# Kernel tuning notes

Measured on AMD Instinct MI355X. Metric: run time of the kernel, lower is better.

The kernel has to match this reference:

```python
import jax, jax.numpy as jnp
import numpy as np
from jax import lax

K = 3          # kernel_size
PAD = 1
D = 2 * K - 2  # 4 trajectory directions
C_IN = 64
C_OUT = 128


def setup_inputs() -> dict:
    key = jax.random.key(0)
    k1, k2, k3, k4, k5 = jax.random.split(key, 5)
    N, C, H, W = 4, C_IN, 128, 128
    x = jax.random.normal(k1, (N, C, H, W), dtype=jnp.float32)
    # conv_offset: Conv2d(C, 2*K*K, K, pad=1, bias=True)
    w_off = jax.random.normal(k2, (2 * K * K, C, K, K), dtype=jnp.float32) * (1.0 / np.sqrt(C * K * K)) * 0.1
    b_off = jax.random.normal(k3, (2 * K * K,), dtype=jnp.float32) * 0.1
    # conv1: DeformConv2d(C, C*D, K, pad=1, groups=C) -> weight (C*D, 1, K, K)
    w_deform = jax.random.normal(k4, (C * D, 1, K, K), dtype=jnp.float32) * (1.0 / np.sqrt(K * K))
    # conv2: 1x1 conv (C*D -> C_OUT), no bias
    w_pw = jax.random.normal(k5, (C_OUT, C * D), dtype=jnp.float32) * (1.0 / np.sqrt(C * D))
    return {"x": x, "w_off": w_off, "b_off": b_off, "w_deform": w_deform, "w_pw": w_pw}


def _deform_sample(x, offsets):
    """Bilinear-sample x at K*K learned-offset locations per output pixel.
    x: (N,C,H,W); offsets: (N, 2*K*K, H, W) with (dy,dx) pairs per kernel tap.
    Returns (N, C, K*K, H, W)."""
    N, C, H, W = x.shape
    kk = K * K
    off = offsets.reshape(N, kk, 2, H, W)
    dy, dx = off[:, :, 0], off[:, :, 1]                    # (N,kk,H,W)
    ky = jnp.repeat(jnp.arange(K), K).astype(jnp.float32)  # (kk,)
    kx = jnp.tile(jnp.arange(K), K).astype(jnp.float32)
    base_y = (jnp.arange(H, dtype=jnp.float32)[None, :, None] - PAD + ky[:, None, None])  # (kk,H,1)
    base_x = (jnp.arange(W, dtype=jnp.float32)[None, None, :] - PAD + kx[:, None, None])  # (kk,1,W)
    py = dy + base_y[None]
    px = dx + base_x[None]
    y0 = jnp.floor(py)
    x0 = jnp.floor(px)
    wy = (py - y0)[:, None]   # (N,1,kk,H,W)
    wx = (px - x0)[:, None]
    y0i = y0.astype(jnp.int32)
    x0i = x0.astype(jnp.int32)
    xf = x.reshape(N, C, H * W)

    def gather(yi, xi):
        valid = ((yi >= 0) & (yi < H) & (xi >= 0) & (xi < W)).astype(x.dtype)
        idx = jnp.clip(yi, 0, H - 1) * W + jnp.clip(xi, 0, W - 1)   # (N,kk,H,W)
        vals = jax.vmap(lambda xn, idxn: xn[:, idxn])(xf, idx)       # (N,C,kk,H,W)
        return vals * valid[:, None]

    v00 = gather(y0i, x0i)
    v01 = gather(y0i, x0i + 1)
    v10 = gather(y0i + 1, x0i)
    v11 = gather(y0i + 1, x0i + 1)
    return (v00 * (1 - wy) * (1 - wx) + v01 * (1 - wy) * wx
            + v10 * wy * (1 - wx) + v11 * wy * wx)


def reference(x, w_off, b_off, w_deform, w_pw):
    N, C, H, W = x.shape
    # conv_offset (3x3, pad 1)
    t = lax.conv_general_dilated(x, w_off, (1, 1), [(PAD, PAD), (PAD, PAD)],
                                 dimension_numbers=("NCHW", "OIHW", "NCHW"))
    t = t + b_off[None, :, None, None]
    # diff_conv with conv_offset: subtract 1x1 conv of x with spatially-summed weight
    ws_off = w_off.sum((2, 3))                               # (2KK, C)
    t = t - jnp.einsum("nchw,oc->nohw", x, ws_off)
    # depthwise deformable conv: sample then contract over kernel taps
    samp = _deform_sample(x, t)                               # (N,C,KK,H,W)
    wd = w_deform.reshape(C, D, K * K)
    y = jnp.einsum("ncphw,cdp->ncdhw", samp, wd).reshape(N, C * D, H, W)
    # diff_conv with conv1 (grouped 1x1: each input channel scales its D outputs)
    ws_d = w_deform.sum((2, 3)).reshape(C, D)
    y = y - jnp.einsum("nchw,cd->ncdhw", x, ws_d).reshape(N, C * D, H, W)
    # pointwise conv2
    return jnp.einsum("nchw,oc->nohw", y, w_pw)
```

## Files before the change

kernel.cpp:

```cpp
#include <hip/hip_runtime.h>

#define DDIM   4
#define CIN    64
#define COUT   128
#define CDIM   256
#define HH     128
#define WWID   128
#define NN     4
#define KK     9
#define OFFC   18
#define HW     (HH * WWID)

#define XS_COLS   73
#define XS_SLICE  (8 * XS_COLS)
#define XS_TOTAL  (8 * XS_SLICE)
#define TL_OFF    XS_TOTAL
#define PART_OFF  (TL_OFF + OFFC * 64)
#define SMEM_FLOATS (PART_OFF + 8 * OFFC * 64)

typedef __attribute__((ext_vector_type(8))) short bf16x8;
typedef __attribute__((ext_vector_type(4))) float f32x4;

__device__ __forceinline__ unsigned short f2bf(float f) {
  union { float f; unsigned u; } c; c.f = f;
  unsigned u = c.u;
  return (unsigned short)((u + 0x7FFFu + ((u >> 16) & 1u)) >> 16);
}

__global__ void convert_wpw(const float* __restrict__ w_pw, unsigned short* __restrict__ wbf) {
  int i = blockIdx.x * 256 + threadIdx.x;
  if (i < COUT * CDIM) wbf[i] = f2bf(w_pw[i]);
}

__global__ __launch_bounds__(512, 4)
void fused_all(const float* __restrict__ x, const float* __restrict__ w_off,
               const float* __restrict__ b_off, const float* __restrict__ w_deform,
               const unsigned short* __restrict__ wbf, float* __restrict__ out) {
  __shared__ float smem[SMEM_FLOATS];

  const int n  = blockIdx.z;
  const int h  = blockIdx.y;
  const int w0 = blockIdx.x * 64;
  const int tid = threadIdx.x;
  const int pl = tid & 63;
  const int cg = tid >> 6;
  const int w = w0 + pl;

  const float* xn = x + (size_t)n * CIN * HW;
  float* xsl  = smem + cg * XS_SLICE;
  float* tl   = smem + TL_OFF;
  float* part = smem + PART_OFF;
  unsigned short* ylds = (unsigned short*)(smem + PART_OFF);

  float ao[OFFC];
#pragma unroll
  for (int o = 0; o < OFFC; ++o) ao[o] = 0.f;

#pragma unroll 1
  for (int ci = 0; ci < 8; ++ci) {
    const int c = __builtin_amdgcn_readfirstlane(cg * 8 + ci);
    const float* xc = xn + (size_t)c * HW;
    for (int i = pl; i < 198; i += 64) {
      int tr = i / 66, tc = i - tr * 66;
      int gy = h - 1 + tr, gx = w0 - 1 + tc;
      float v = 0.f;
      if (gy >= 0 && gy < HH && gx >= 0 && gx < WWID) v = xc[gy * WWID + gx];
      xsl[tr * 66 + tc] = v;
    }
    const float center = xsl[66 + pl + 1];
    float v[KK];
#pragma unroll
    for (int p = 0; p < KK; ++p)
      v[p] = xsl[(p / 3) * 66 + pl + (p % 3)] - center;
#pragma unroll
    for (int o = 0; o < OFFC; ++o) {
      const float* wrow = w_off + ((size_t)o * CIN + c) * KK;
      float a = ao[o];
#pragma unroll
      for (int p = 0; p < KK; ++p) {
        if (p == 4) continue;
        a += wrow[p] * v[p];
      }
      ao[o] = a;
    }
  }
#pragma unroll
  for (int o = 0; o < OFFC; ++o) part[(cg * OFFC + o) * 64 + pl] = ao[o];
  __syncthreads();

  for (int idx = tid; idx < OFFC * 64; idx += 512) {
    const int o = idx >> 6, px = idx & 63;
    float s = b_off[o];
#pragma unroll
    for (int w8 = 0; w8 < 8; ++w8) s += part[(w8 * OFFC + o) * 64 + px];
    tl[o * 64 + px] = s;
  }
  __syncthreads();

  const int row0 = min(max(h - 3, 0), HH - 8);
  const int col0 = min(max(w0 - 3, 0), WWID - 72);
  const int hc  = h - row0;
  const int wcb = w0 - col0;
  unsigned pk[KK];
  float c00[KK], c01[KK], c10[KK], c11[KK];
  unsigned inmask = 0;
#pragma unroll
  for (int p = 0; p < KK; ++p) {
    const float dy = tl[(2 * p) * 64 + pl];
    const float dx = tl[(2 * p + 1) * 64 + pl];
    const float py  = dy + (float)(h + p / 3 - 1);
    const float pxx = dx + (float)(w + p % 3 - 1);
    const float fy = floorf(py), fx = floorf(pxx);
    const int y0 = (int)fy, x0 = (int)fx;
    const int y1 = y0 + 1,  x1 = x0 + 1;
    const float ay = py - fy, ax = pxx - fx;
    const bool vy0 = (y0 >= 0) && (y0 < HH), vy1 = (y1 >= 0) && (y1 < HH);
    const bool vx0 = (x0 >= 0) && (x0 < WWID), vx1 = (x1 >= 0) && (x1 < WWID);
    const int yc0 = min(max(y0, 0), HH - 1),  yc1 = min(max(y1, 0), HH - 1);
    const int xc0 = min(max(x0, 0), WWID - 1), xc1 = min(max(x1, 0), WWID - 1);
    const int ty0 = yc0 - row0, ty1 = yc1 - row0;
    const int tx0 = xc0 - col0, tx1 = xc1 - col0;
    if ((unsigned)ty0 < 8u && (unsigned)ty1 < 8u && (unsigned)tx0 < 72u && (unsigned)tx1 < 72u)
      inmask |= 1u << p;
    pk[p] = (unsigned)(ty0 & 255) | ((unsigned)(ty1 & 255) << 8)
          | ((unsigned)(tx0 & 255) << 16) | ((unsigned)(tx1 & 255) << 24);
    c00[p] = (vy0 && vx0) ? (1.f - ay) * (1.f - ax) : 0.f;
    c01[p] = (vy0 && vx1) ? (1.f - ay) * ax         : 0.f;
    c10[p] = (vy1 && vx0) ? ay * (1.f - ax)         : 0.f;
    c11[p] = (vy1 && vx1) ? ay * ax                 : 0.f;
  }

#pragma unroll 1
  for (int ci = 0; ci < 8; ++ci) {
    const int c = __builtin_amdgcn_readfirstlane(cg * 8 + ci);
    const float* xc = xn + (size_t)c * HW;
#pragma unroll
    for (int k = 0; k < 9; ++k) {
      const int i = pl + k * 64;
      const int r = i / 72, cl = i - r * 72;
      xsl[r * XS_COLS + cl] = xc[(row0 + r) * WWID + col0 + cl];
    }
    const float xcv = xsl[hc * XS_COLS + pl + wcb];
    float yd0 = 0.f, yd1 = 0.f, yd2 = 0.f, yd3 = 0.f;
#pragma unroll
    for (int p = 0; p < KK; ++p) {
      float samp;
      if (inmask & (1u << p)) {
        const unsigned k4 = pk[p];
        const int ty0 = k4 & 255, ty1 = (k4 >> 8) & 255;
        const int tx0 = (k4 >> 16) & 255, tx1 = k4 >> 24;
        samp = c00[p] * xsl[ty0 * XS_COLS + tx0] + c01[p] * xsl[ty0 * XS_COLS + tx1]
             + c10[p] * xsl[ty1 * XS_COLS + tx0] + c11[p] * xsl[ty1 * XS_COLS + tx1];
      } else {
        const float dy = tl[(2 * p) * 64 + pl];
        const float dx = tl[(2 * p + 1) * 64 + pl];
        const float py  = dy + (float)(h + p / 3 - 1);
        const float pxx = dx + (float)(w + p % 3 - 1);
        const float fy = floorf(py), fx = floorf(pxx);
        const int y0 = (int)fy, x0 = (int)fx;
        const int yc0 = min(max(y0, 0), HH - 1),  yc1 = min(max(y0 + 1, 0), HH - 1);
        const int xc0 = min(max(x0, 0), WWID - 1), xc1 = min(max(x0 + 1, 0), WWID - 1);
        samp = c00[p] * xc[yc0 * WWID + xc0] + c01[p] * xc[yc0 * WWID + xc1]
             + c10[p] * xc[yc1 * WWID + xc0] + c11[p] * xc[yc1 * WWID + xc1];
      }
      const float s = samp - xcv;
      const float* wdp = w_deform + (size_t)(c * DDIM) * KK + p;
      yd0 += wdp[0 * KK] * s;
      yd1 += wdp[1 * KK] * s;
      yd2 += wdp[2 * KK] * s;
      yd3 += wdp[3 * KK] * s;
    }
    const unsigned lo = (unsigned)f2bf(yd0) | ((unsigned)f2bf(yd1) << 16);
    const unsigned hi = (unsigned)f2bf(yd2) | ((unsigned)f2bf(yd3) << 16);
    const int ebase = (((c >> 1) ^ (pl & 7)) << 3) + (c & 1) * 4;
    *reinterpret_cast<uint2*>(&ylds[pl * CDIM + ebase]) = make_uint2(lo, hi);
  }
  __syncthreads();

  const int l15 = tid & 15;
  const int kg  = (tid & 63) >> 4;
  const int Mb = (cg >> 1) * 32;
  const int Nb = (cg & 1) * 32;

  f32x4 acc[2][2];
#pragma unroll
  for (int mi = 0; mi < 2; ++mi)
#pragma unroll
    for (int ni = 0; ni < 2; ++ni)
      acc[mi][ni] = (f32x4){0.f, 0.f, 0.f, 0.f};

#pragma unroll
  for (int ks = 0; ks < 8; ++ks) {
    bf16x8 bfr[2];
#pragma unroll
    for (int ni = 0; ni < 2; ++ni) {
      const int prow = Nb + ni * 16 + l15;
      const int chunk = ks * 4 + kg;
      const int eb = ((chunk ^ (prow & 7)) << 3);
      bfr[ni] = *reinterpret_cast<const bf16x8*>(&ylds[prow * CDIM + eb]);
    }
    bf16x8 afr[2];
#pragma unroll
    for (int mi = 0; mi < 2; ++mi) {
      const int o = Mb + mi * 16 + l15;
      afr[mi] = *reinterpret_cast<const bf16x8*>(wbf + (size_t)o * CDIM + ks * 32 + kg * 8);
    }
#pragma unroll
    for (int mi = 0; mi < 2; ++mi)
#pragma unroll
      for (int ni = 0; ni < 2; ++ni)
        acc[mi][ni] = __builtin_amdgcn_mfma_f32_16x16x32_bf16(afr[mi], bfr[ni], acc[mi][ni], 0, 0, 0);
  }

  float* on = out + (size_t)n * COUT * HW;
#pragma unroll
  for (int mi = 0; mi < 2; ++mi) {
#pragma unroll
    for (int ni = 0; ni < 2; ++ni) {
      const int pcol = h * WWID + w0 + Nb + ni * 16 + l15;
#pragma unroll
      for (int reg = 0; reg < 4; ++reg) {
        const int o = Mb + mi * 16 + kg * 4 + reg;
        on[(size_t)o * HW + pcol] = acc[mi][ni][reg];
      }
    }
  }
}

extern "C" void kernel_launch(void* const* d_in, const int* in_sizes, int n_in,
                              void* d_out, int out_size, void* d_ws, size_t ws_size,
                              hipStream_t stream) {
  const float* x        = (const float*)d_in[0];
  const float* w_off    = (const float*)d_in[1];
  const float* b_off    = (const float*)d_in[2];
  const float* w_deform = (const float*)d_in[3];
  const float* w_pw     = (const float*)d_in[4];
  float* out = (float*)d_out;
  unsigned short* wbf = (unsigned short*)d_ws;

  convert_wpw<<<dim3(COUT * CDIM / 256), dim3(256), 0, stream>>>(w_pw, wbf);
  fused_all<<<dim3(WWID / 64, HH, NN), dim3(512), 0, stream>>>(x, w_off, b_off, w_deform, wbf, out);
}
```

Before: 179.1 us.

## Software-pipeline channel tile loads through registers and swizzle block order

Both the offset-conv and deformable-sampling channel loops now prefetch the next channel's tile into registers while computing the current one, with global indices precomputed once. The sampling tile shrinks from 8 to 7 rows so the LDS footprint drops, and the partial offset sums are stored as bf16 so they fit in the y buffer. Block indices are remapped so consecutive blocks land on different (n,h) groups, which changes cache locality. This trades extra registers and reduced offset precision for hidden global load latency and less LDS; there appears to be no barrier between writing the tile and reading it from other lanes, so wave-local LDS hazards depend on each slice being private to one wave.

```diff
diff --git a/kernel.cpp b/kernel.cpp
--- a/kernel.cpp
+++ b/kernel.cpp
@@ -11,20 +11,25 @@
 #define OFFC   18
 #define HW     (HH * WWID)
 
-#define XS_COLS   73
-#define XS_SLICE  (8 * XS_COLS)
+#define XS_SLICE  511
 #define XS_TOTAL  (8 * XS_SLICE)
 #define TL_OFF    XS_TOTAL
-#define PART_OFF  (TL_OFF + OFFC * 64)
-#define SMEM_FLOATS (PART_OFF + 8 * OFFC * 64)
+#define YL_OFF    (TL_OFF + OFFC * 64)
+#define SMEM_FLOATS (YL_OFF + 8192)
 
 typedef __attribute__((ext_vector_type(8))) short bf16x8;
 typedef __attribute__((ext_vector_type(4))) float f32x4;
+
+#define RFL(x) __builtin_amdgcn_readfirstlane(x)
 
 __device__ __forceinline__ unsigned short f2bf(float f) {
   union { float f; unsigned u; } c; c.f = f;
   unsigned u = c.u;
   return (unsigned short)((u + 0x7FFFu + ((u >> 16) & 1u)) >> 16);
+}
+__device__ __forceinline__ float bf2f(unsigned short u) {
+  union { unsigned u; float f; } c; c.u = (unsigned)u << 16;
+  return c.f;
 }
 
 __global__ void convert_wpw(const float* __restrict__ w_pw, unsigned short* __restrict__ wbf) {
@@ -38,35 +43,50 @@
                const unsigned short* __restrict__ wbf, float* __restrict__ out) {
   __shared__ float smem[SMEM_FLOATS];
 
-  const int n  = blockIdx.z;
-  const int h  = blockIdx.y;
-  const int w0 = blockIdx.x * 64;
+  const int lin = blockIdx.x + 2 * blockIdx.y + 256 * blockIdx.z;
+  const int swz = ((lin & 7) << 7) + (lin >> 3);
+  const int n  = swz >> 8;
+  const int h  = (swz >> 1) & 127;
+  const int w0 = (swz & 1) * 64;
+
   const int tid = threadIdx.x;
   const int pl = tid & 63;
   const int cg = tid >> 6;
   const int w = w0 + pl;
 
   const float* xn = x + (size_t)n * CIN * HW;
-  float* xsl  = smem + cg * XS_SLICE;
-  float* tl   = smem + TL_OFF;
-  float* part = smem + PART_OFF;
-  unsigned short* ylds = (unsigned short*)(smem + PART_OFF);
+  float* xsl = smem + cg * XS_SLICE;
+  float* tl  = smem + TL_OFF;
+  unsigned short* pt   = (unsigned short*)(smem + YL_OFF);
+  unsigned short* ylds = (unsigned short*)(smem + YL_OFF);
 
   float ao[OFFC];
 #pragma unroll
   for (int o = 0; o < OFFC; ++o) ao[o] = 0.f;
 
-#pragma unroll 1
-  for (int ci = 0; ci < 8; ++ci) {
-    const int c = __builtin_amdgcn_readfirstlane(cg * 8 + ci);
+  int g0[4]; unsigned okm = 0;
+#pragma unroll
+  for (int k = 0; k < 4; ++k) {
+    const int i = pl + k * 64;
+    const int tr = i / 66, tc = i - tr * 66;
+    const int gy = h - 1 + tr, gx = w0 - 1 + tc;
+    const bool ok = (i < 198) && gy >= 0 && gy < HH && gx >= 0 && gx < WWID;
+    g0[k] = ok ? (gy * WWID + gx) : 0;
+    okm |= ok ? (1u << k) : 0u;
+  }
+  auto p0_load = [&](float* b, int c) {
     const float* xc = xn + (size_t)c * HW;
-    for (int i = pl; i < 198; i += 64) {
-      int tr = i / 66, tc = i - tr * 66;
-      int gy = h - 1 + tr, gx = w0 - 1 + tc;
-      float v = 0.f;
-      if (gy >= 0 && gy < HH && gx >= 0 && gx < WWID) v = xc[gy * WWID + gx];
-      xsl[tr * 66 + tc] = v;
-    }
+#pragma unroll
+    for (int k = 0; k < 4; ++k) b[k] = ((okm >> k) & 1) ? xc[g0[k]] : 0.f;
+  };
+  auto p0_write = [&](const float* b) {
+#pragma unroll
+    for (int k = 0; k < 4; ++k) {
+      if (k < 3) xsl[pl + k * 64] = b[k];
+      else if (pl < 6) xsl[pl + 192] = b[3];
+    }
+  };
+  auto p0_comp = [&](int c) {
     const float center = xsl[66 + pl + 1];
     float v[KK];
 #pragma unroll
@@ -83,21 +103,35 @@
       }
       ao[o] = a;
     }
-  }
-#pragma unroll
-  for (int o = 0; o < OFFC; ++o) part[(cg * OFFC + o) * 64 + pl] = ao[o];
+  };
+
+  {
+    float pA[4], pB[4];
+    p0_load(pA, RFL(cg * 8));
+#pragma unroll
+    for (int c2 = 0; c2 < 8; c2 += 2) {
+      p0_write(pA);
+      p0_load(pB, RFL(cg * 8 + c2 + 1));
+      p0_comp(RFL(cg * 8 + c2));
+      p0_write(pB);
+      if (c2 < 6) p0_load(pA, RFL(cg * 8 + c2 + 2));
+      p0_comp(RFL(cg * 8 + c2 + 1));
+    }
+  }
+#pragma unroll
+  for (int o = 0; o < OFFC; ++o) pt[(cg * OFFC + o) * 64 + pl] = f2bf(ao[o]);
   __syncthreads();
 
   for (int idx = tid; idx < OFFC * 64; idx += 512) {
     const int o = idx >> 6, px = idx & 63;
     float s = b_off[o];
 #pragma unroll
-    for (int w8 = 0; w8 < 8; ++w8) s += part[(w8 * OFFC + o) * 64 + px];
+    for (int w8 = 0; w8 < 8; ++w8) s += bf2f(pt[(w8 * OFFC + o) * 64 + px]);
     tl[o * 64 + px] = s;
   }
   __syncthreads();
 
-  const int row0 = min(max(h - 3, 0), HH - 8);
+  const int row0 = min(max(h - 3, 0), HH - 7);
   const int col0 = min(max(w0 - 3, 0), WWID - 72);
   const int hc  = h - row0;
   const int wcb = w0 - col0;
@@ -120,7 +154,7 @@
     const int xc0 = min(max(x0, 0), WWID - 1), xc1 = min(max(x1, 0), WWID - 1);
     const int ty0 = yc0 - row0, ty1 = yc1 - row0;
     const int tx0 = xc0 - col0, tx1 = xc1 - col0;
-    if ((unsigned)ty0 < 8u && (unsigned)ty1 < 8u && (unsigned)tx0 < 72u && (unsigned)tx1 < 72u)
+    if ((unsigned)ty0 < 7u && (unsigned)ty1 < 7u && (unsigned)tx0 < 72u && (unsigned)tx1 < 72u)
       inmask |= 1u << p;
     pk[p] = (unsigned)(ty0 & 255) | ((unsigned)(ty1 & 255) << 8)
           | ((unsigned)(tx0 & 255) << 16) | ((unsigned)(tx1 & 255) << 24);
@@ -130,17 +164,32 @@
     c11[p] = (vy1 && vx1) ? ay * ax                 : 0.f;
   }
 
-#pragma unroll 1
-  for (int ci = 0; ci < 8; ++ci) {
-    const int c = __builtin_amdgcn_readfirstlane(cg * 8 + ci);
+  int g1[8], l1[8];
+#pragma unroll
+  for (int k = 0; k < 8; ++k) {
+    const int i = pl + k * 64;
+    const int r = i / 72, cl = i - r * 72;
+    g1[k] = (row0 + r) * WWID + col0 + cl;
+    l1[k] = r * 73 + cl;
+  }
+  auto p1_load = [&](float* b, int c) {
     const float* xc = xn + (size_t)c * HW;
 #pragma unroll
-    for (int k = 0; k < 9; ++k) {
-      const int i = pl + k * 64;
-      const int r = i / 72, cl = i - r * 72;
-      xsl[r * XS_COLS + cl] = xc[(row0 + r) * WWID + col0 + cl];
-    }
-    const float xcv = xsl[hc * XS_COLS + pl + wcb];
+    for (int k = 0; k < 8; ++k) {
+      if (k < 7) b[k] = xc[g1[k]];
+      else if (pl < 56) b[7] = xc[g1[7]];
+    }
+  };
+  auto p1_write = [&](const float* b) {
+#pragma unroll
+    for (int k = 0; k < 8; ++k) {
+      if (k < 7) xsl[l1[k]] = b[k];
+      else if (pl < 56) xsl[l1[7]] = b[7];
+    }
+  };
+  auto p1_comp = [&](int c) {
+    const float* xc = xn + (size_t)c * HW;
+    const float xcv = xsl[hc * 73 + wcb + pl];
     float yd0 = 0.f, yd1 = 0.f, yd2 = 0.f, yd3 = 0.f;
 #pragma unroll
     for (int p = 0; p < KK; ++p) {
@@ -149,8 +198,8 @@
         const unsigned k4 = pk[p];
         const int ty0 = k4 & 255, ty1 = (k4 >> 8) & 255;
         const int tx0 = (k4 >> 16) & 255, tx1 = k4 >> 24;
-        samp = c00[p] * xsl[ty0 * XS_COLS + tx0] + c01[p] * xsl[ty0 * XS_COLS + tx1]
-             + c10[p] * xsl[ty1 * XS_COLS + tx0] + c11[p] * xsl[ty1 * XS_COLS + tx1];
+        samp = c00[p] * xsl[ty0 * 73 + tx0] + c01[p] * xsl[ty0 * 73 + tx1]
+             + c10[p] * xsl[ty1 * 73 + tx0] + c11[p] * xsl[ty1 * 73 + tx1];
       } else {
         const float dy = tl[(2 * p) * 64 + pl];
         const float dx = tl[(2 * p + 1) * 64 + pl];
@@ -174,6 +223,20 @@
     const unsigned hi = (unsigned)f2bf(yd2) | ((unsigned)f2bf(yd3) << 16);
     const int ebase = (((c >> 1) ^ (pl & 7)) << 3) + (c & 1) * 4;
     *reinterpret_cast<uint2*>(&ylds[pl * CDIM + ebase]) = make_uint2(lo, hi);
+  };
+
+  {
+    float qA[8], qB[8];
+    p1_load(qA, RFL(cg * 8));
+#pragma unroll
+    for (int c2 = 0; c2 < 8; c2 += 2) {
+      p1_write(qA);
+      p1_load(qB, RFL(cg * 8 + c2 + 1));
+      p1_comp(RFL(cg * 8 + c2));
+      p1_write(qB);
+      if (c2 < 6) p1_load(qA, RFL(cg * 8 + c2 + 2));
+      p1_comp(RFL(cg * 8 + c2 + 1));
+    }
   }
   __syncthreads();
 
```

Result: slower. 326.1 us (+82.1%).
